# Kernel tuning notes

Hardware: AMD Instinct MI355X
Metric: run time of the kernel (lower is better)

## Reference

```python
import jax, jax.numpy as jnp
import numpy as np

SCALES = (0, 1, 2, 3)
SIGMA_NSQ = 2.0
SIGMA_MAX_INV = 4.0 / (255.0 * 255.0)
GAIN_LIMIT = 100.0  # NEG=False
EPS = 1e-10


def gaussian_kernel_2d(N):
    sigma = N / 5.0
    x = jnp.arange(N, dtype=jnp.float32) - (N - 1) / 2.0
    g = jnp.exp(-(x * x) / (2.0 * sigma * sigma))
    k = jnp.outer(g, g)
    return (k / jnp.sum(k))[None, None]  # [1,1,N,N]


def reflect_pad(x, p):
    return jnp.pad(x, ((0, 0), (0, 0), (p, p), (p, p)), mode='reflect')


def conv2d(x, w, stride=1, groups=1):
    return jax.lax.conv_general_dilated(
        x, w, (stride, stride), 'VALID',
        dimension_numbers=('NCHW', 'OIHW', 'NCHW'),
        feature_group_count=groups)


def vif_num_den(ref, dist):
    ref = ref - 128.0
    dist = dist - 128.0
    h, w = ref.shape[-2], ref.shape[-1]
    nums, dens = [], []
    for scale in SCALES:
        N = 2 ** (4 - scale) + 1
        win = gaussian_kernel_2d(N)
        p = (N - 1) // 2
        if scale > 0:
            h, w = h // 2, w // 2
            ref = conv2d(reflect_pad(ref, p), win, stride=2)[:, :, :h, :w]
            dist = conv2d(reflect_pad(dist, p), win, stride=2)[:, :, :h, :w]
        win5 = jnp.tile(win, (5, 1, 1, 1))  # grouped conv, 5 channels
        inp = jnp.concatenate([ref, dist, ref * ref, dist * dist, ref * dist], axis=1)
        out = conv2d(reflect_pad(inp, p), win5, groups=5)  # [b,5,h,w]
        mu1, mu2, s1, s2, s12 = [out[:, i:i + 1] for i in range(5)]
        s1 = jax.nn.relu(s1 - mu1 * mu1)
        s2 = jax.nn.relu(s2 - mu2 * mu2)
        s12 = s12 - mu1 * mu2
        g = s12 / (s1 + EPS)
        sv = s2 - g * s12
        m1 = s1 < EPS
        g = jnp.where(m1, 0.0, g)
        sv = jnp.where(m1, s2, sv)
        s1 = jnp.where(m1, 0.0, s1)
        m2 = s2 < EPS
        g = jnp.where(m2, 0.0, g)
        sv = jnp.where(m2, 0.0, sv)
        sv = jnp.where(g < 0.0, s2, sv)
        g = jax.nn.relu(g)
        sv = jnp.where(sv <= EPS, EPS, sv)
        g = jnp.minimum(g, GAIN_LIMIT)
        num_ar = jnp.log2(1.0 + g * g * s1 / (sv + SIGMA_NSQ))
        den_ar = jnp.log2(1.0 + s1 / SIGMA_NSQ)
        num_ar = jnp.where(s12 < 0.0, 0.0, num_ar)
        m3 = s1 < SIGMA_NSQ
        num_ar = jnp.where(m3, 1.0 - s2 * SIGMA_MAX_INV, num_ar)
        den_ar = jnp.where(m3, 1.0, den_ar)
        nums.append(jnp.sum(num_ar, axis=(-1, -2, -3)))
        dens.append(jnp.sum(den_ar, axis=(-1, -2, -3)))
    return jnp.stack(nums, axis=-1), jnp.stack(dens, axis=-1)


def setup_inputs() -> dict:
    key = jax.random.key(0)
    k1, k2 = jax.random.split(key)
    shape = (4, 1, 1080, 1920)
    ref = jax.random.uniform(k1, shape, dtype=jnp.float32) * 255.0
    dist = jax.random.uniform(k2, shape, dtype=jnp.float32) * 255.0
    return {"ref": ref, "dist": dist}


def reference(ref, dist):
    num, den = vif_num_den(ref, dist)
    return num / den  # VIF features per scale, shape [b, 4]
```

## Files before the change

kernel.cpp:

```cpp
#include <hip/hip_runtime.h>
#include <math.h>

#define VIF_EPS       1e-10f
#define SIGMA_NSQ     2.0f
#define SIGMA_MAX_INV (4.0f / (255.0f * 255.0f))
#define GAIN_LIMIT    100.0f

typedef float v2f __attribute__((ext_vector_type(2)));
typedef float v4f __attribute__((ext_vector_type(4)));

static __device__ __forceinline__ v2f splat2(float s) {
    v2f v; v.x = s; v.y = s; return v;
}

__device__ __forceinline__ int reflect_idx(int i, int n) {
    i = (i < 0) ? -i : i;
    i = (i >= n) ? (2 * n - 2 - i) : i;
    return i;
}

template <int N>
__device__ __forceinline__ void fill_weights_global(float* gw) {
    const float sigma = (float)N / 5.0f;
    const float denom = 2.0f * sigma * sigma;
    float tmp[N];
    float s = 0.0f;
    for (int i = 0; i < N; ++i) {
        float x = (float)i - (float)(N - 1) * 0.5f;
        float g = expf(-(x * x) / denom);
        tmp[i] = g;
        s += g;
    }
    for (int i = 0; i < N; ++i) gw[i] = tmp[i] / s;
}

__global__ __launch_bounds__(64) void init_weights_kernel(float* __restrict__ gw,
                                                          unsigned* __restrict__ counter) {
    const int tid = threadIdx.x;
    if (tid == 0) fill_weights_global<17>(gw + 0);
    else if (tid == 1) fill_weights_global<9>(gw + 17);
    else if (tid == 2) fill_weights_global<5>(gw + 26);
    else if (tid == 3) fill_weights_global<3>(gw + 31);
    else if (tid == 4) *counter = 0u;
}

__host__ __device__ constexpr int w_off(int N) {
    return (N == 17) ? 0 : (N == 9) ? 17 : (N == 5) ? 26 : 31;
}

constexpr int tile_w(int N) { return (256 - (N - 1)) & ~3; }

template <int N>
struct alignas(16) StatsSmem {
    v2f   a[8][256];
    v2f   bq[8][256];
    float c[8][256];
};
template <int N>
struct alignas(16) DownSmem {
    v2f vb[8][252];
};

template <int N>
__device__ __forceinline__ void stats_body(
    StatsSmem<N>& sm, const float* __restrict__ refp, const float* __restrict__ distp,
    const float* __restrict__ gw,
    int h, int w, float shift, double2* __restrict__ partial,
    int sy, int sx, int bx, int b) {
    constexpr int P   = (N - 1) / 2;
    constexpr int TW  = tile_w(N);
    constexpr int TH  = 8;
    constexpr int LR  = TH + 2 * P;
    constexpr int XG4 = TW / 4;
    constexpr int NT  = TH * XG4;
    constexpr int REPS = (NT + 255) / 256;

    const int tid = threadIdx.x;
    const int ytile = bx % sy;
    const int xtile = bx / sy;
    const int x0 = xtile * TW;
    const int y0 = ytile * TH;

    float wr[N];
#pragma unroll
    for (int j = 0; j < N; ++j) wr[j] = gw[j];

    {
        const int cc = tid;
        const int gx = reflect_idx(x0 + cc - P, w);
        const float* rbase = refp  + (size_t)b * h * w;
        const float* dbase = distp + (size_t)b * h * w;

        v2f accA[TH], accB[TH];
        float accC[TH];
#pragma unroll
        for (int t = 0; t < TH; ++t) {
            accA[t] = splat2(0.f);
            accB[t] = splat2(0.f);
            accC[t] = 0.f;
        }

        auto acc_push = [&](int i, float r, float d) {
            v2f rd; rd.x = r; rd.y = d;
            v2f sq = rd * rd;
            float x = r * d;
#pragma unroll
            for (int t = 0; t < TH; ++t) {
                const int j = i - t;
                if (j >= 0 && j < N) {
                    const float wj = wr[j];
                    accA[t] += splat2(wj) * rd;
                    accB[t] += splat2(wj) * sq;
                    accC[t] += wj * x;
                }
            }
        };

        const int rowlo = y0 - P;
        if (rowlo >= 0 && rowlo + LR <= h) {
            unsigned voff = (unsigned)(rowlo * w + gx) * 4u;
            const unsigned vstep = (unsigned)w * 4u;
#pragma unroll
            for (int i = 0; i < LR; ++i) {
                float r = *(const float*)((const char*)rbase + voff) - shift;
                float d = *(const float*)((const char*)dbase + voff) - shift;
                voff += vstep;
                acc_push(i, r, d);
            }
        } else {
#pragma unroll
            for (int i = 0; i < LR; ++i) {
                const int gy = reflect_idx(rowlo + i, h);
                const size_t o = (size_t)gy * w + gx;
                float r = rbase[o] - shift;
                float d = dbase[o] - shift;
                acc_push(i, r, d);
            }
        }
#pragma unroll
        for (int t = 0; t < TH; ++t) {
            sm.a[t][cc]  = accA[t];
            sm.bq[t][cc] = accB[t];
            sm.c[t][cc]  = accC[t];
        }
    }
    __syncthreads();

    float num_v = 0.f, den_v = 0.f;
    {
        constexpr int WC  = N + 3;
        constexpr int F4C = (WC + 3) / 4;
#pragma unroll
        for (int rep = 0; rep < REPS; ++rep) {
            const int task = tid + 256 * rep;
            if (task < NT) {
                const int row = task / XG4;
                const int xg  = task - row * XG4;

                v2f muA[4], muB[4];
                float muC[4];
#pragma unroll
                for (int q = 0; q < 4; ++q) {
                    muA[q] = splat2(0.f);
                    muB[q] = splat2(0.f);
                    muC[q] = 0.f;
                }

                const v4f* A4 = (const v4f*)&sm.a[row][xg * 4];
                const v4f* B4 = (const v4f*)&sm.bq[row][xg * 4];
#pragma unroll
                for (int f = 0; f < WC / 2; ++f) {
                    v4f ta = A4[f];
                    v4f tb = B4[f];
#pragma unroll
                    for (int hlf = 0; hlf < 2; ++hlf) {
                        const int k = 2 * f + hlf;
                        v2f pa = hlf ? __builtin_shufflevector(ta, ta, 2, 3)
                                     : __builtin_shufflevector(ta, ta, 0, 1);
                        v2f pb = hlf ? __builtin_shufflevector(tb, tb, 2, 3)
                                     : __builtin_shufflevector(tb, tb, 0, 1);
#pragma unroll
                        for (int q = 0; q < 4; ++q) {
                            const int j = k - q;
                            if (j >= 0 && j < N) {
                                const float wj = wr[j];
                                muA[q] += splat2(wj) * pa;
                                muB[q] += splat2(wj) * pb;
                            }
                        }
                    }
                }
                {
                    const v4f* C4 = (const v4f*)&sm.c[row][xg * 4];
#pragma unroll
                    for (int f = 0; f < F4C; ++f) {
                        v4f t = C4[f];
#pragma unroll
                        for (int e = 0; e < 4; ++e) {
                            const int k = 4 * f + e;
                            const float x = (e == 0) ? t.x : (e == 1) ? t.y
                                          : (e == 2) ? t.z : t.w;
#pragma unroll
                            for (int q = 0; q < 4; ++q) {
                                const int j = k - q;
                                if (j >= 0 && j < N) muC[q] += wr[j] * x;
                            }
                        }
                    }
                }

                const int gy = y0 + row;
#pragma unroll
                for (int q = 0; q < 4; ++q) {
                    int gx = x0 + xg * 4 + q;
                    if (gx < w && gy < h) {
                        float mu1 = muA[q].x, mu2 = muA[q].y;
                        float s1  = fmaxf(0.f, muB[q].x - mu1 * mu1);
                        float s2  = fmaxf(0.f, muB[q].y - mu2 * mu2);
                        float s12 = muC[q] - mu1 * mu2;

                        float g  = s12 / (s1 + VIF_EPS);
                        float sv = s2 - g * s12;
                        if (s1 < VIF_EPS) { g = 0.f; sv = s2; s1 = 0.f; }
                        if (s2 < VIF_EPS) { g = 0.f; sv = 0.f; }
                        if (g  < 0.f)     { sv = s2; g = 0.f; }
                        if (sv <= VIF_EPS) sv = VIF_EPS;
                        g = fminf(g, GAIN_LIMIT);

                        float num_ar = __log2f(1.f + g * g * s1 / (sv + SIGMA_NSQ));
                        float den_ar = __log2f(1.f + s1 / SIGMA_NSQ);
                        if (s12 < 0.f) num_ar = 0.f;
                        if (s1 < SIGMA_NSQ) { num_ar = 1.f - s2 * SIGMA_MAX_INV; den_ar = 1.f; }
                        num_v += num_ar;
                        den_v += den_ar;
                    }
                }
            }
        }
    }

#pragma unroll
    for (int off = 32; off > 0; off >>= 1) {
        num_v += __shfl_down(num_v, off);
        den_v += __shfl_down(den_v, off);
    }
    __syncthreads();
    float* rs = reinterpret_cast<float*>(&sm);
    const int wid = tid >> 6, lane = tid & 63;
    if (lane == 0) { rs[wid] = num_v; rs[4 + wid] = den_v; }
    __syncthreads();
    if (tid == 0) {
        float ns = rs[0] + rs[1] + rs[2] + rs[3];
        float ds = rs[4] + rs[5] + rs[6] + rs[7];
        partial[(size_t)b * (sy * sx) + bx] = make_double2((double)ns, (double)ds);
    }
}

template <int N>
__device__ __forceinline__ void down_body(
    DownSmem<N>& sm, const float* __restrict__ rin, const float* __restrict__ din,
    const float* __restrict__ gw,
    float* __restrict__ rout, float* __restrict__ dout,
    int h, int w, int h2, int w2, float shift, int dgx, int bx, int b) {
    constexpr int P   = (N - 1) / 2;
    constexpr int TOW = 120, TOH = 8;
    constexpr int IC  = 2 * (TOW - 1) + N;
    constexpr int NR  = 2 * (TOH - 1) + N;
    constexpr int XG4 = TOW / 4;
    constexpr int WL  = N + 6;

    float wr[N];
#pragma unroll
    for (int j = 0; j < N; ++j) wr[j] = gw[j];

    const int tid = threadIdx.x;
    const int xt  = bx % dgx;
    const int yt  = bx / dgx;
    const int x0  = xt * TOW;
    const int y0  = yt * TOH;

    if (tid < IC) {
        const int gx = reflect_idx(2 * x0 - P + tid, w);
        const int rowlo = 2 * y0 - P;
        const float* rbase = rin + (size_t)b * h * w;
        const float* dbase = din + (size_t)b * h * w;

        v2f acc[TOH];
#pragma unroll
        for (int t = 0; t < TOH; ++t) acc[t] = splat2(0.f);

        const bool interior = (rowlo >= 0) && (rowlo + NR <= h);
        if (interior) {
            unsigned voff = (unsigned)(rowlo * w + gx) * 4u;
            const unsigned vstep = (unsigned)w * 4u;
#pragma unroll
            for (int i = 0; i < NR; ++i) {
                v2f x;
                x.x = *(const float*)((const char*)rbase + voff) - shift;
                x.y = *(const float*)((const char*)dbase + voff) - shift;
                voff += vstep;
#pragma unroll
                for (int t = 0; t < TOH; ++t) {
                    const int j = i - 2 * t;
                    if (j >= 0 && j < N) acc[t] += splat2(wr[j]) * x;
                }
            }
        } else {
#pragma unroll
            for (int i = 0; i < NR; ++i) {
                const int gy = reflect_idx(rowlo + i, h);
                const size_t o = (size_t)gy * w + gx;
                v2f x; x.x = rbase[o] - shift; x.y = dbase[o] - shift;
#pragma unroll
                for (int t = 0; t < TOH; ++t) {
                    const int j = i - 2 * t;
                    if (j >= 0 && j < N) acc[t] += splat2(wr[j]) * x;
                }
            }
        }
#pragma unroll
        for (int t = 0; t < TOH; ++t) sm.vb[t][tid] = acc[t];
    }
    __syncthreads();

    if (tid < TOH * XG4) {
        const int row = tid / XG4;
        const int xg  = tid - row * XG4;

        v2f o[4];
#pragma unroll
        for (int q = 0; q < 4; ++q) o[q] = splat2(0.f);

        const v4f* s4 = (const v4f*)&sm.vb[row][8 * xg];
#pragma unroll
        for (int f = 0; f < (WL + 1) / 2; ++f) {
            v4f t = s4[f];
#pragma unroll
            for (int hlf = 0; hlf < 2; ++hlf) {
                const int k = 2 * f + hlf;
                v2f p = hlf ? __builtin_shufflevector(t, t, 2, 3)
                            : __builtin_shufflevector(t, t, 0, 1);
#pragma unroll
                for (int q = 0; q < 4; ++q) {
                    const int j = k - 2 * q;
                    if (j >= 0 && j < N) o[q] += splat2(wr[j]) * p;
                }
            }
        }
        const int gy = y0 + row;
        if (gy < h2) {
            float* rp = rout + (size_t)b * h2 * w2 + (size_t)gy * w2 + x0 + 4 * xg;
            float* dp = dout + (size_t)b * h2 * w2 + (size_t)gy * w2 + x0 + 4 * xg;
            *(float4*)rp = make_float4(o[0].x, o[1].x, o[2].x, o[3].x);
            *(float4*)dp = make_float4(o[0].y, o[1].y, o[2].y, o[3].y);
        }
    }
}

template <int NS, int ND>
__global__ __launch_bounds__(256) void fused_kernel(
    const float* __restrict__ sref, const float* __restrict__ sdist,
    const float* __restrict__ gw,
    int sh, int sw, float sshift, double2* __restrict__ partial, int sy, int sx,
    float* __restrict__ drout, float* __restrict__ ddout,
    int dh2, int dw2, int dgx, int nStats) {
    __shared__ union {
        StatsSmem<NS> s;
        DownSmem<ND>  d;
    } u;
    const int bx = blockIdx.x;
    const int b  = blockIdx.z;
    if (bx < nStats)
        stats_body<NS>(u.s, sref, sdist, gw + w_off(NS), sh, sw, sshift,
                       partial, sy, sx, bx, b);
    else
        down_body<ND>(u.d, sref, sdist, gw + w_off(ND), drout, ddout,
                      sh, sw, dh2, dw2, sshift, dgx, bx - nStats, b);
}

template <int N>
__global__ __launch_bounds__(256) void stats_reduce_kernel(
    const float* __restrict__ refp, const float* __restrict__ distp,
    const float* __restrict__ gw,
    int h, int w, float shift, double2* __restrict__ partial, int sy, int sx,
    unsigned* __restrict__ counter,
    const double2* __restrict__ part, float* __restrict__ out,
    int4 bases, int4 counts) {
    __shared__ StatsSmem<N> sm;
    __shared__ unsigned slast;
    __shared__ double sn[4], sd[4];

    stats_body<N>(sm, refp, distp, gw + w_off(N), h, w, shift, partial,
                  sy, sx, blockIdx.x, blockIdx.z);

    __threadfence();
    if (threadIdx.x == 0) {
        const unsigned total = gridDim.x * gridDim.z;
        unsigned old = atomicAdd(counter, 1u);
        slast = (old == total - 1u) ? 1u : 0u;
    }
    __syncthreads();
    if (!slast) return;

    __threadfence();
    const int tid = threadIdx.x;
    for (int v = 0; v < 16; ++v) {
        const int s = v & 3;
        const int b = v >> 2;
        const int base = (&bases.x)[s];
        const int cnt  = (&counts.x)[s];
        const double2* p = part + base + (size_t)b * cnt;

        double ns = 0.0, ds = 0.0;
        for (int i = tid; i < cnt; i += 256) {
            double2 t = p[i];
            ns += t.x;
            ds += t.y;
        }
#pragma unroll
        for (int off = 32; off > 0; off >>= 1) {
            ns += __shfl_down(ns, off);
            ds += __shfl_down(ds, off);
        }
        const int wid = tid >> 6, lane = tid & 63;
        if (lane == 0) { sn[wid] = ns; sd[wid] = ds; }
        __syncthreads();
        if (tid == 0) {
            double Nv = sn[0] + sn[1] + sn[2] + sn[3];
            double Dv = sd[0] + sd[1] + sd[2] + sd[3];
            out[b * 4 + s] = (float)(Nv / Dv);
        }
        __syncthreads();
    }
}

extern "C" void kernel_launch(void* const* d_in, const int* in_sizes, int n_in,
                              void* d_out, int out_size, void* d_ws, size_t ws_size,
                              hipStream_t stream) {
    const float* ref  = (const float*)d_in[0];
    const float* dist = (const float*)d_in[1];
    float* out = (float*)d_out;

    const int B = 4;
    const int H0 = 1080, W0 = 1920;
    const int H1 = 540,  W1 = 960;
    const int H2 = 270,  W2 = 480;
    const int H3 = 135,  W3 = 240;

    char*  ws  = (char*)d_ws;
    size_t off = 0;
    auto alloc = [&](size_t bytes) -> void* {
        void* p = ws + off;
        off += (bytes + 255) & ~(size_t)255;
        return p;
    };
    float*    gw      = (float*)alloc(34 * sizeof(float));
    unsigned* counter = (unsigned*)alloc(sizeof(unsigned));
    float* ref1  = (float*)alloc((size_t)B * H1 * W1 * 4);
    float* dist1 = (float*)alloc((size_t)B * H1 * W1 * 4);
    float* ref2  = (float*)alloc((size_t)B * H2 * W2 * 4);
    float* dist2 = (float*)alloc((size_t)B * H2 * W2 * 4);
    float* ref3  = (float*)alloc((size_t)B * H3 * W3 * 4);
    float* dist3 = (float*)alloc((size_t)B * H3 * W3 * 4);

    const int sx0 = (W0 + tile_w(17) - 1) / tile_w(17), sy0 = (H0 + 7) / 8;
    const int sx1 = (W1 + tile_w(9)  - 1) / tile_w(9),  sy1 = (H1 + 7) / 8;
    const int sx2 = (W2 + tile_w(5)  - 1) / tile_w(5),  sy2 = (H2 + 7) / 8;
    const int sx3 = (W3 + tile_w(3)  - 1) / tile_w(3),  sy3 = (H3 + 7) / 8;
    const int n0 = sx0 * sy0, n1 = sx1 * sy1, n2 = sx2 * sy2, n3 = sx3 * sy3;

    const int dgx1 = W1 / 120, nD1 = dgx1 * ((H1 + 7) / 8);
    const int dgx2 = W2 / 120, nD2 = dgx2 * ((H2 + 7) / 8);
    const int dgx3 = W3 / 120, nD3 = dgx3 * ((H3 + 7) / 8);

    double2* part = (double2*)alloc((size_t)B * (n0 + n1 + n2 + n3) * sizeof(double2));
    double2* p0 = part;
    double2* p1 = p0 + (size_t)B * n0;
    double2* p2 = p1 + (size_t)B * n1;
    double2* p3 = p2 + (size_t)B * n2;

    dim3 blk(256);

    init_weights_kernel<<<1, 64, 0, stream>>>(gw, counter);

    fused_kernel<17, 9><<<dim3(n0 + nD1, 1, B), blk, 0, stream>>>(
        ref, dist, gw, H0, W0, 128.0f, p0, sy0, sx0,
        ref1, dist1, H1, W1, dgx1, n0);

    fused_kernel<9, 5><<<dim3(n1 + nD2, 1, B), blk, 0, stream>>>(
        ref1, dist1, gw, H1, W1, 0.0f, p1, sy1, sx1,
        ref2, dist2, H2, W2, dgx2, n1);

    fused_kernel<5, 3><<<dim3(n2 + nD3, 1, B), blk, 0, stream>>>(
        ref2, dist2, gw, H2, W2, 0.0f, p2, sy2, sx2,
        ref3, dist3, H3, W3, dgx3, n2);

    stats_reduce_kernel<3><<<dim3(n3, 1, B), blk, 0, stream>>>(
        ref3, dist3, gw, H3, W3, 0.0f, p3, sy3, sx3,
        counter, part, out,
        make_int4(0, B * n0, B * (n0 + n1), B * (n0 + n1 + n2)),
        make_int4(n0, n1, n2, n3));
}
```

Before: 193.7 us.

## Merge level-2 stats, level-3 downsample and final reduction into one kernel

Replaces the last two launches (level-2 stats plus level-3 downsample, then level-3 stats plus final reduction) with a single kernel. Level-3 blocks rebuild their downsampled input patch in shared memory straight from the level-2 image, recomputing the 3-tap downsample locally instead of writing level-3 images to global memory. The final reduction is also restructured to load all partials in unrolled passes with constants. This removes a launch and a round trip through global memory, at the cost of hardcoded sizes and some redundant downsample work per block.

```diff
diff --git a/kernel.cpp b/kernel.cpp
--- a/kernel.cpp
+++ b/kernel.cpp
@@ -60,10 +60,18 @@
 struct alignas(16) DownSmem {
     v2f vb[8][252];
 };
-
-template <int N>
+struct alignas(16) Stats3Smem {
+    union {
+        StatsSmem<3> planes;
+        v2f vb3[10][481];
+    } u2;
+    v2f patch[10][240];
+};
+
+template <int N, bool FROM_PATCH>
 __device__ __forceinline__ void stats_body(
     StatsSmem<N>& sm, const float* __restrict__ refp, const float* __restrict__ distp,
+    const v2f* __restrict__ patch,
     const float* __restrict__ gw,
     int h, int w, float shift, double2* __restrict__ partial,
     int sy, int sx, int bx, int b) {
@@ -88,8 +96,6 @@
     {
         const int cc = tid;
         const int gx = reflect_idx(x0 + cc - P, w);
-        const float* rbase = refp  + (size_t)b * h * w;
-        const float* dbase = distp + (size_t)b * h * w;
 
         v2f accA[TH], accB[TH];
         float accC[TH];
@@ -116,25 +122,35 @@
             }
         };
 
-        const int rowlo = y0 - P;
-        if (rowlo >= 0 && rowlo + LR <= h) {
-            unsigned voff = (unsigned)(rowlo * w + gx) * 4u;
-            const unsigned vstep = (unsigned)w * 4u;
+        if constexpr (FROM_PATCH) {
 #pragma unroll
             for (int i = 0; i < LR; ++i) {
-                float r = *(const float*)((const char*)rbase + voff) - shift;
-                float d = *(const float*)((const char*)dbase + voff) - shift;
-                voff += vstep;
-                acc_push(i, r, d);
+                v2f pv = patch[i * 240 + gx];
+                acc_push(i, pv.x, pv.y);
             }
         } else {
-#pragma unroll
-            for (int i = 0; i < LR; ++i) {
-                const int gy = reflect_idx(rowlo + i, h);
-                const size_t o = (size_t)gy * w + gx;
-                float r = rbase[o] - shift;
-                float d = dbase[o] - shift;
-                acc_push(i, r, d);
+            const float* rbase = refp  + (size_t)b * h * w;
+            const float* dbase = distp + (size_t)b * h * w;
+            const int rowlo = y0 - P;
+            if (rowlo >= 0 && rowlo + LR <= h) {
+                unsigned voff = (unsigned)(rowlo * w + gx) * 4u;
+                const unsigned vstep = (unsigned)w * 4u;
+#pragma unroll
+                for (int i = 0; i < LR; ++i) {
+                    float r = *(const float*)((const char*)rbase + voff) - shift;
+                    float d = *(const float*)((const char*)dbase + voff) - shift;
+                    voff += vstep;
+                    acc_push(i, r, d);
+                }
+            } else {
+#pragma unroll
+                for (int i = 0; i < LR; ++i) {
+                    const int gy = reflect_idx(rowlo + i, h);
+                    const size_t o = (size_t)gy * w + gx;
+                    float r = rbase[o] - shift;
+                    float d = dbase[o] - shift;
+                    acc_push(i, r, d);
+                }
             }
         }
 #pragma unroll
@@ -371,52 +387,124 @@
     const int bx = blockIdx.x;
     const int b  = blockIdx.z;
     if (bx < nStats)
-        stats_body<NS>(u.s, sref, sdist, gw + w_off(NS), sh, sw, sshift,
-                       partial, sy, sx, bx, b);
+        stats_body<NS, false>(u.s, sref, sdist, nullptr, gw + w_off(NS), sh, sw,
+                              sshift, partial, sy, sx, bx, b);
     else
         down_body<ND>(u.d, sref, sdist, gw + w_off(ND), drout, ddout,
                       sh, sw, dh2, dw2, sshift, dgx, bx - nStats, b);
 }
 
-template <int N>
-__global__ __launch_bounds__(256) void stats_reduce_kernel(
-    const float* __restrict__ refp, const float* __restrict__ distp,
+__device__ __forceinline__ void build_l3_patch(
+    v2f* __restrict__ vb3 , v2f* __restrict__ patch ,
+    const float* __restrict__ r2, const float* __restrict__ d2,
+    const float* __restrict__ gw3, int y0, int b) {
+    constexpr int H2v = 270, W2v = 480, H3v = 135;
+    const int tid = threadIdx.x;
+    const float w0 = gw3[0], w1 = gw3[1], w2 = gw3[2];
+    const float* rb = r2 + (size_t)b * H2v * W2v;
+    const float* db = d2 + (size_t)b * H2v * W2v;
+
+#pragma unroll
+    for (int rep = 0; rep < 2; ++rep) {
+        const int t = tid + 256 * rep;
+        if (t < 481) {
+            const int c2 = reflect_idx(t - 1, W2v);
+#pragma unroll
+            for (int py = 0; py < 10; ++py) {
+                const int y3  = reflect_idx(y0 - 1 + py, H3v);
+                const int r0  = reflect_idx(2 * y3 - 1, H2v);
+                const int r1  = 2 * y3;
+                const int r2i = 2 * y3 + 1;
+                v2f m = splat2(0.f);
+                v2f x;
+                x.x = rb[(size_t)r0 * W2v + c2];  x.y = db[(size_t)r0 * W2v + c2];
+                m += splat2(w0) * x;
+                x.x = rb[(size_t)r1 * W2v + c2];  x.y = db[(size_t)r1 * W2v + c2];
+                m += splat2(w1) * x;
+                x.x = rb[(size_t)r2i * W2v + c2]; x.y = db[(size_t)r2i * W2v + c2];
+                m += splat2(w2) * x;
+                vb3[py * 481 + t] = m;
+            }
+        }
+    }
+    __syncthreads();
+#pragma unroll
+    for (int rep = 0; rep < 10; ++rep) {
+        const int idx = tid + 256 * rep;
+        if (idx < 2400) {
+            const int py = idx / 240;
+            const int x3 = idx - py * 240;
+            v2f o = splat2(0.f);
+            o += splat2(w0) * vb3[py * 481 + 2 * x3 + 0];
+            o += splat2(w1) * vb3[py * 481 + 2 * x3 + 1];
+            o += splat2(w2) * vb3[py * 481 + 2 * x3 + 2];
+            patch[py * 240 + x3] = o;
+        }
+    }
+    __syncthreads();
+}
+
+constexpr int RN0 = 1080, RN1 = 272, RN2 = 68, RN3 = 17;
+constexpr int RB0 = 0, RB1 = 4 * RN0, RB2 = 4 * (RN0 + RN1), RB3 = 4 * (RN0 + RN1 + RN2);
+
+__global__ __launch_bounds__(256) void level23_kernel(
+    const float* __restrict__ ref2, const float* __restrict__ dist2,
     const float* __restrict__ gw,
-    int h, int w, float shift, double2* __restrict__ partial, int sy, int sx,
+    double2* __restrict__ p2, double2* __restrict__ p3,
     unsigned* __restrict__ counter,
-    const double2* __restrict__ part, float* __restrict__ out,
-    int4 bases, int4 counts) {
-    __shared__ StatsSmem<N> sm;
+    const double2* __restrict__ part, float* __restrict__ out) {
+    __shared__ union {
+        StatsSmem<5> s5;
+        Stats3Smem   s3;
+    } u;
     __shared__ unsigned slast;
     __shared__ double sn[4], sd[4];
 
-    stats_body<N>(sm, refp, distp, gw + w_off(N), h, w, shift, partial,
-                  sy, sx, blockIdx.x, blockIdx.z);
+    const int bx  = blockIdx.x;
+    const int b   = blockIdx.z;
+    const int tid = threadIdx.x;
+
+    if (bx < 68) {
+        stats_body<5, false>(u.s5, ref2, dist2, nullptr, gw + w_off(5),
+                             270, 480, 0.f, p2, 34, 2, bx, b);
+    } else {
+        const int bx3 = bx - 68;
+        build_l3_patch(&u.s3.u2.vb3[0][0], &u.s3.patch[0][0],
+                       ref2, dist2, gw + w_off(3), bx3 * 8, b);
+        stats_body<3, true>(u.s3.u2.planes, nullptr, nullptr, &u.s3.patch[0][0],
+                            gw + w_off(3), 135, 240, 0.f, p3, 17, 1, bx3, b);
+    }
 
     __threadfence();
-    if (threadIdx.x == 0) {
+    if (tid == 0) {
         const unsigned total = gridDim.x * gridDim.z;
-        unsigned old = atomicAdd(counter, 1u);
-        slast = (old == total - 1u) ? 1u : 0u;
+        slast = (atomicAdd(counter, 1u) == total - 1u) ? 1u : 0u;
     }
     __syncthreads();
     if (!slast) return;
-
     __threadfence();
-    const int tid = threadIdx.x;
+
+    const int cntv[4]  = {RN0, RN1, RN2, RN3};
+    const int basev[4] = {RB0, RB1, RB2, RB3};
+    double accn[16], accd[16];
+#pragma unroll
+    for (int v = 0; v < 16; ++v) { accn[v] = 0.0; accd[v] = 0.0; }
+#pragma unroll
+    for (int k = 0; k < 5; ++k) {
+#pragma unroll
+        for (int v = 0; v < 16; ++v) {
+            const int s = v & 3, bb = v >> 2;
+            const int i = tid + 256 * k;
+            if (i < cntv[s]) {
+                double2 t = part[basev[s] + (size_t)bb * cntv[s] + i];
+                accn[v] += t.x;
+                accd[v] += t.y;
+            }
+        }
+    }
+#pragma unroll
     for (int v = 0; v < 16; ++v) {
-        const int s = v & 3;
-        const int b = v >> 2;
-        const int base = (&bases.x)[s];
-        const int cnt  = (&counts.x)[s];
-        const double2* p = part + base + (size_t)b * cnt;
-
-        double ns = 0.0, ds = 0.0;
-        for (int i = tid; i < cnt; i += 256) {
-            double2 t = p[i];
-            ns += t.x;
-            ds += t.y;
-        }
+        double ns = accn[v], ds = accd[v];
 #pragma unroll
         for (int off = 32; off > 0; off >>= 1) {
             ns += __shfl_down(ns, off);
@@ -428,7 +516,7 @@
         if (tid == 0) {
             double Nv = sn[0] + sn[1] + sn[2] + sn[3];
             double Dv = sd[0] + sd[1] + sd[2] + sd[3];
-            out[b * 4 + s] = (float)(Nv / Dv);
+            out[(v >> 2) * 4 + (v & 3)] = (float)(Nv / Dv);
         }
         __syncthreads();
     }
@@ -445,7 +533,6 @@
     const int H0 = 1080, W0 = 1920;
     const int H1 = 540,  W1 = 960;
     const int H2 = 270,  W2 = 480;
-    const int H3 = 135,  W3 = 240;
 
     char*  ws  = (char*)d_ws;
     size_t off = 0;
@@ -460,24 +547,20 @@
     float* dist1 = (float*)alloc((size_t)B * H1 * W1 * 4);
     float* ref2  = (float*)alloc((size_t)B * H2 * W2 * 4);
     float* dist2 = (float*)alloc((size_t)B * H2 * W2 * 4);
-    float* ref3  = (float*)alloc((size_t)B * H3 * W3 * 4);
-    float* dist3 = (float*)alloc((size_t)B * H3 * W3 * 4);
 
     const int sx0 = (W0 + tile_w(17) - 1) / tile_w(17), sy0 = (H0 + 7) / 8;
     const int sx1 = (W1 + tile_w(9)  - 1) / tile_w(9),  sy1 = (H1 + 7) / 8;
-    const int sx2 = (W2 + tile_w(5)  - 1) / tile_w(5),  sy2 = (H2 + 7) / 8;
-    const int sx3 = (W3 + tile_w(3)  - 1) / tile_w(3),  sy3 = (H3 + 7) / 8;
-    const int n0 = sx0 * sy0, n1 = sx1 * sy1, n2 = sx2 * sy2, n3 = sx3 * sy3;
+    const int n0 = sx0 * sy0;
+    const int n1 = sx1 * sy1;
 
     const int dgx1 = W1 / 120, nD1 = dgx1 * ((H1 + 7) / 8);
     const int dgx2 = W2 / 120, nD2 = dgx2 * ((H2 + 7) / 8);
-    const int dgx3 = W3 / 120, nD3 = dgx3 * ((H3 + 7) / 8);
-
-    double2* part = (double2*)alloc((size_t)B * (n0 + n1 + n2 + n3) * sizeof(double2));
+
+    double2* part = (double2*)alloc((size_t)B * (RN0 + RN1 + RN2 + RN3) * sizeof(double2));
     double2* p0 = part;
-    double2* p1 = p0 + (size_t)B * n0;
-    double2* p2 = p1 + (size_t)B * n1;
-    double2* p3 = p2 + (size_t)B * n2;
+    double2* p1 = p0 + (size_t)B * RN0;
+    double2* p2 = p1 + (size_t)B * RN1;
+    double2* p3 = p2 + (size_t)B * RN2;
 
     dim3 blk(256);
 
@@ -491,13 +574,6 @@
         ref1, dist1, gw, H1, W1, 0.0f, p1, sy1, sx1,
         ref2, dist2, H2, W2, dgx2, n1);
 
-    fused_kernel<5, 3><<<dim3(n2 + nD3, 1, B), blk, 0, stream>>>(
-        ref2, dist2, gw, H2, W2, 0.0f, p2, sy2, sx2,
-        ref3, dist3, H3, W3, dgx3, n2);
-
-    stats_reduce_kernel<3><<<dim3(n3, 1, B), blk, 0, stream>>>(
-        ref3, dist3, gw, H3, W3, 0.0f, p3, sy3, sx3,
-        counter, part, out,
-        make_int4(0, B * n0, B * (n0 + n1), B * (n0 + n1 + n2)),
-        make_int4(n0, n1, n2, n3));
-}
+    level23_kernel<<<dim3(68 + 17, 1, B), blk, 0, stream>>>(
+        ref2, dist2, gw, p2, p3, counter, part, out);
+}
```

Measured after the change: 204.1 us. 5.3% more time.
